# Kernel tuning notes

Measured on AMD Instinct MI355X. Metric: run time of the kernel, lower is better.

## Reference

```python
import jax, jax.numpy as jnp
import numpy as np

EMBED_DIM = 768
NUM_HEADS = 12
HEAD_DIM = EMBED_DIM // NUM_HEADS
SCALE = HEAD_DIM ** -0.5
B, S = 4, 2048


def setup_inputs() -> dict:
    key = jax.random.key(0)
    ks = jax.random.split(key, 9)
    w = 0.02
    return {
        "hidden_states": jax.random.normal(ks[0], (B, S, EMBED_DIM), jnp.float32),
        "Wq": jax.random.normal(ks[1], (EMBED_DIM, EMBED_DIM), jnp.float32) * w,
        "bq": jax.random.normal(ks[2], (EMBED_DIM,), jnp.float32) * w,
        "Wk": jax.random.normal(ks[3], (EMBED_DIM, EMBED_DIM), jnp.float32) * w,
        "bk": jax.random.normal(ks[4], (EMBED_DIM,), jnp.float32) * w,
        "Wv": jax.random.normal(ks[5], (EMBED_DIM, EMBED_DIM), jnp.float32) * w,
        "bv": jax.random.normal(ks[6], (EMBED_DIM,), jnp.float32) * w,
        "Wo": jax.random.normal(ks[7], (EMBED_DIM, EMBED_DIM), jnp.float32) * w,
        "bo": jax.random.normal(ks[8], (EMBED_DIM,), jnp.float32) * w,
    }


def reference(hidden_states, Wq, bq, Wk, bk, Wv, bv, Wo, bo):
    b, s, _ = hidden_states.shape
    # projections (torch Linear: x @ W.T + b)
    q = hidden_states @ Wq.T + bq
    k = hidden_states @ Wk.T + bk
    v = hidden_states @ Wv.T + bv
    # [b, h, s, d]
    q = q.reshape(b, s, NUM_HEADS, HEAD_DIM).transpose(0, 2, 1, 3)
    k = k.reshape(b, s, NUM_HEADS, HEAD_DIM).transpose(0, 2, 1, 3)
    v = v.reshape(b, s, NUM_HEADS, HEAD_DIM).transpose(0, 2, 1, 3)
    # full [b, h, s, s] attention matrix (faithful to the original, no fusion)
    attn_weights = jnp.einsum("bhqd,bhkd->bhqk", q, k) * SCALE
    attn_weights = jax.nn.softmax(attn_weights, axis=-1)
    attn_output = jnp.einsum("bhqk,bhkd->bhqd", attn_weights, v)
    attn_output = attn_output.transpose(0, 2, 1, 3).reshape(b, s, EMBED_DIM)
    attn_output = attn_output @ Wo.T + bo
    return attn_output, attn_weights
```

## Files before the change

kernel.cpp:

```cpp
#include <hip/hip_runtime.h>
#include <hip/hip_bf16.h>
#include <stdint.h>

#define EMBED 768
#define NH    12
#define HD    64
#define BB    4
#define SSEQ  2048
#define TOK   (BB*SSEQ)
#define ATT_SCALE 0.125f

typedef short  short8  __attribute__((ext_vector_type(8)));
typedef float  floatx4 __attribute__((ext_vector_type(4)));

__device__ __forceinline__ unsigned short f2bf(float f) {
  unsigned int u = __float_as_uint(f);
  return (unsigned short)((u + 0x7fffu + ((u >> 16) & 1u)) >> 16);
}

__device__ __forceinline__ void gl_lds16(const void* gsrc, void* ldst) {
  __builtin_amdgcn_global_load_lds(
      (__attribute__((address_space(1))) void*)(uintptr_t)gsrc,
      (__attribute__((address_space(3))) void*)ldst, 16, 0, 0);
}

__global__ void cvtk(const float* __restrict__ x, unsigned short* __restrict__ y, int n4) {
  int i = blockIdx.x * blockDim.x + threadIdx.x;
  if (i < n4) {
    float4 v = ((const float4*)x)[i];
    ushort4 o;
    o.x = f2bf(v.x); o.y = f2bf(v.y); o.z = f2bf(v.z); o.w = f2bf(v.w);
    ((ushort4*)y)[i] = o;
  }
}

__global__ __launch_bounds__(256, 2) void gemm_qkv(
    const unsigned short* __restrict__ Xb,
    const unsigned short* __restrict__ Wqb, const unsigned short* __restrict__ Wkb,
    const unsigned short* __restrict__ Wvb,
    const float* __restrict__ bq, const float* __restrict__ bk, const float* __restrict__ bv,
    unsigned short* __restrict__ Qw, unsigned short* __restrict__ Kw,
    unsigned short* __restrict__ Vw)
{
  __shared__ __align__(16) unsigned short As[128*64];
  __shared__ __align__(16) unsigned short Bs[128*64];
  const int z = blockIdx.z;
  const unsigned short* Wb = (z == 0) ? Wqb : (z == 1) ? Wkb : Wvb;
  const float* bias        = (z == 0) ? bq  : (z == 1) ? bk  : bv;
  unsigned short* Out      = (z == 0) ? Qw  : (z == 1) ? Kw  : Vw;

  const int tid = threadIdx.x;
  const int wid = tid >> 6, lane = tid & 63, quad = lane >> 4, l15 = lane & 15;
  const int wm = (wid >> 1) * 64, wn = (wid & 1) * 64;
  const int m0 = blockIdx.y * 128, n0 = blockIdx.x * 128;

  floatx4 acc[4][4] = {};

  for (int k0 = 0; k0 < EMBED; k0 += 64) {
#pragma unroll
    for (int p = 0; p < 4; ++p) {
      int f = p*256 + tid;
      int row = f >> 3, ch = f & 7;
      gl_lds16(Xb + (size_t)(m0+row)*EMBED + k0 + ch*8, &As[f*8]);
      gl_lds16(Wb + (size_t)(n0+row)*EMBED + k0 + ch*8, &Bs[f*8]);
    }
    __syncthreads();
#pragma unroll
    for (int kk = 0; kk < 2; ++kk) {
      short8 af[4], bf[4];
#pragma unroll
      for (int i = 0; i < 4; ++i)
        af[i] = *(const short8*)&As[(wm + i*16 + l15)*64 + kk*32 + quad*8];
#pragma unroll
      for (int j = 0; j < 4; ++j)
        bf[j] = *(const short8*)&Bs[(wn + j*16 + l15)*64 + kk*32 + quad*8];
#pragma unroll
      for (int i = 0; i < 4; ++i)
#pragma unroll
        for (int j = 0; j < 4; ++j)
          acc[i][j] = __builtin_amdgcn_mfma_f32_16x16x32_bf16(af[i], bf[j], acc[i][j], 0, 0, 0);
    }
    __syncthreads();
  }

#pragma unroll
  for (int j = 0; j < 4; ++j) {
    int n = n0 + wn + j*16 + l15;
    float bia = bias[n];
    int h = n >> 6, d = n & 63;
#pragma unroll
    for (int i = 0; i < 4; ++i) {
#pragma unroll
      for (int r = 0; r < 4; ++r) {
        int m = m0 + wm + i*16 + quad*4 + r;
        int b = m >> 11, s = m & 2047;
        Out[(size_t)(b*NH + h)*SSEQ*HD + (size_t)s*HD + d] = f2bf(acc[i][j][r] + bia);
      }
    }
  }
}

__global__ __launch_bounds__(256, 2) void gemm_o(
    const unsigned short* __restrict__ Ab, const unsigned short* __restrict__ Wb,
    const float* __restrict__ bias, float* __restrict__ Fo)
{
  __shared__ __align__(16) unsigned short As[128*64];
  __shared__ __align__(16) unsigned short Bs[128*64];
  const int tid = threadIdx.x;
  const int wid = tid >> 6, lane = tid & 63, quad = lane >> 4, l15 = lane & 15;
  const int wm = (wid >> 1) * 64, wn = (wid & 1) * 64;
  const int m0 = blockIdx.y * 128, n0 = blockIdx.x * 128;

  floatx4 acc[4][4] = {};

  for (int k0 = 0; k0 < EMBED; k0 += 64) {
#pragma unroll
    for (int p = 0; p < 4; ++p) {
      int f = p*256 + tid;
      int row = f >> 3, ch = f & 7;
      gl_lds16(Ab + (size_t)(m0+row)*EMBED + k0 + ch*8, &As[f*8]);
      gl_lds16(Wb + (size_t)(n0+row)*EMBED + k0 + ch*8, &Bs[f*8]);
    }
    __syncthreads();
#pragma unroll
    for (int kk = 0; kk < 2; ++kk) {
      short8 af[4], bf[4];
#pragma unroll
      for (int i = 0; i < 4; ++i)
        af[i] = *(const short8*)&As[(wm + i*16 + l15)*64 + kk*32 + quad*8];
#pragma unroll
      for (int j = 0; j < 4; ++j)
        bf[j] = *(const short8*)&Bs[(wn + j*16 + l15)*64 + kk*32 + quad*8];
#pragma unroll
      for (int i = 0; i < 4; ++i)
#pragma unroll
        for (int j = 0; j < 4; ++j)
          acc[i][j] = __builtin_amdgcn_mfma_f32_16x16x32_bf16(af[i], bf[j], acc[i][j], 0, 0, 0);
    }
    __syncthreads();
  }

#pragma unroll
  for (int j = 0; j < 4; ++j) {
    int n = n0 + wn + j*16 + l15;
    float bia = bias[n];
#pragma unroll
    for (int i = 0; i < 4; ++i) {
#pragma unroll
      for (int r = 0; r < 4; ++r) {
        int m = m0 + wm + i*16 + quad*4 + r;
        Fo[(size_t)m*EMBED + n] = acc[i][j][r] + bia;
      }
    }
  }
}

__global__ __launch_bounds__(256, 2) void attn(
    const unsigned short* __restrict__ Qw, const unsigned short* __restrict__ Kw,
    const unsigned short* __restrict__ Vw, unsigned short* __restrict__ AP,
    float* __restrict__ AWout)
{
  __shared__ __align__(16) unsigned short Qs[128*64];
  __shared__ __align__(16) unsigned short Ks[64*64];
  __shared__ __align__(16) unsigned short Vt[64*72];
  __shared__ __align__(16) unsigned short Ps[128*72];
  const int tid = threadIdx.x;
  const int wid = tid >> 6, lane = tid & 63, quad = lane >> 4, l15 = lane & 15;
  const int bh = blockIdx.x;
  const int q0 = blockIdx.y * 128;
  const unsigned short* Qh = Qw + (size_t)bh * SSEQ * HD;
  const unsigned short* Kh = Kw + (size_t)bh * SSEQ * HD;
  const unsigned short* Vh = Vw + (size_t)bh * SSEQ * HD;
  float* aw = AWout + (size_t)bh * SSEQ * SSEQ + (size_t)q0 * SSEQ;

#pragma unroll
  for (int p = 0; p < 4; ++p) {
    int f = p*256 + tid;
    gl_lds16(Qh + (size_t)(q0 + (f >> 3))*HD + (f & 7)*8, &Qs[f*8]);
  }

  float mi[2][4], li[2][4];
#pragma unroll
  for (int mf = 0; mf < 2; ++mf)
#pragma unroll
    for (int r = 0; r < 4; ++r) { mi[mf][r] = -1e30f; li[mf][r] = 0.f; }

  for (int kt = 0; kt < SSEQ/64; ++kt) {
    int k0 = kt * 64;
#pragma unroll
    for (int p = 0; p < 2; ++p) {
      int f = p*256 + tid;
      gl_lds16(Kh + (size_t)(k0 + (f >> 3))*HD + (f & 7)*8, &Ks[f*8]);
    }
    __syncthreads();

    floatx4 sa[2][4] = {};
#pragma unroll
    for (int kk = 0; kk < 2; ++kk) {
      short8 qf[2], kf[4];
#pragma unroll
      for (int mf = 0; mf < 2; ++mf)
        qf[mf] = *(const short8*)&Qs[(wid*32 + mf*16 + l15)*64 + kk*32 + quad*8];
#pragma unroll
      for (int nf = 0; nf < 4; ++nf)
        kf[nf] = *(const short8*)&Ks[(nf*16 + l15)*64 + kk*32 + quad*8];
#pragma unroll
      for (int mf = 0; mf < 2; ++mf)
#pragma unroll
        for (int nf = 0; nf < 4; ++nf)
          sa[mf][nf] = __builtin_amdgcn_mfma_f32_16x16x32_bf16(qf[mf], kf[nf], sa[mf][nf], 0, 0, 0);
    }
#pragma unroll
    for (int mf = 0; mf < 2; ++mf) {
#pragma unroll
      for (int r = 0; r < 4; ++r) {
        float s0 = sa[mf][0][r]*ATT_SCALE, s1 = sa[mf][1][r]*ATT_SCALE;
        float s2 = sa[mf][2][r]*ATT_SCALE, s3 = sa[mf][3][r]*ATT_SCALE;
        float tm = fmaxf(fmaxf(s0, s1), fmaxf(s2, s3));
#pragma unroll
        for (int msk = 1; msk < 16; msk <<= 1) tm = fmaxf(tm, __shfl_xor(tm, msk, 16));
        float mn = fmaxf(mi[mf][r], tm);
        float se = __expf(s0-mn) + __expf(s1-mn) + __expf(s2-mn) + __expf(s3-mn);
#pragma unroll
        for (int msk = 1; msk < 16; msk <<= 1) se += __shfl_xor(se, msk, 16);
        li[mf][r] = li[mf][r]*__expf(mi[mf][r]-mn) + se;
        mi[mf][r] = mn;
      }
    }
    __syncthreads();
  }

  float rli[2][4];
#pragma unroll
  for (int mf = 0; mf < 2; ++mf)
#pragma unroll
    for (int r = 0; r < 4; ++r) rli[mf][r] = 1.0f / li[mf][r];

  floatx4 oa[2][4] = {};
  for (int kt = 0; kt < SSEQ/64; ++kt) {
    int k0 = kt * 64;
#pragma unroll
    for (int p = 0; p < 2; ++p) {
      int f = p*256 + tid;
      gl_lds16(Kh + (size_t)(k0 + (f >> 3))*HD + (f & 7)*8, &Ks[f*8]);
    }
#pragma unroll
    for (int p = 0; p < 2; ++p) {
      int j = p*32 + (tid >> 3);
      int ch = tid & 7;
      short8 v = *(const short8*)&Vh[(size_t)(k0 + j)*HD + ch*8];
#pragma unroll
      for (int i = 0; i < 8; ++i)
        Vt[(ch*8 + i)*72 + j] = (unsigned short)v[i];
    }
    __syncthreads();

    floatx4 sa[2][4] = {};
#pragma unroll
    for (int kk = 0; kk < 2; ++kk) {
      short8 qf[2], kf[4];
#pragma unroll
      for (int mf = 0; mf < 2; ++mf)
        qf[mf] = *(const short8*)&Qs[(wid*32 + mf*16 + l15)*64 + kk*32 + quad*8];
#pragma unroll
      for (int nf = 0; nf < 4; ++nf)
        kf[nf] = *(const short8*)&Ks[(nf*16 + l15)*64 + kk*32 + quad*8];
#pragma unroll
      for (int mf = 0; mf < 2; ++mf)
#pragma unroll
        for (int nf = 0; nf < 4; ++nf)
          sa[mf][nf] = __builtin_amdgcn_mfma_f32_16x16x32_bf16(qf[mf], kf[nf], sa[mf][nf], 0, 0, 0);
    }

#pragma unroll
    for (int mf = 0; mf < 2; ++mf) {
#pragma unroll
      for (int nf = 0; nf < 4; ++nf) {
#pragma unroll
        for (int r = 0; r < 4; ++r) {
          float p = __expf(sa[mf][nf][r]*ATT_SCALE - mi[mf][r]) * rli[mf][r];
          int rl = wid*32 + mf*16 + quad*4 + r;
          aw[(size_t)rl*SSEQ + k0 + nf*16 + l15] = p;
          Ps[rl*72 + nf*16 + l15] = f2bf(p);
        }
      }
    }
#pragma unroll
    for (int kk = 0; kk < 2; ++kk) {
      short8 pf[2], vf[4];
#pragma unroll
      for (int mf = 0; mf < 2; ++mf)
        pf[mf] = *(const short8*)&Ps[(wid*32 + mf*16 + l15)*72 + kk*32 + quad*8];
#pragma unroll
      for (int nd = 0; nd < 4; ++nd)
        vf[nd] = *(const short8*)&Vt[(nd*16 + l15)*72 + kk*32 + quad*8];
#pragma unroll
      for (int mf = 0; mf < 2; ++mf)
#pragma unroll
        for (int nd = 0; nd < 4; ++nd)
          oa[mf][nd] = __builtin_amdgcn_mfma_f32_16x16x32_bf16(pf[mf], vf[nd], oa[mf][nd], 0, 0, 0);
    }
    __syncthreads();
  }

  const int b = bh / NH, h = bh % NH;
#pragma unroll
  for (int mf = 0; mf < 2; ++mf) {
#pragma unroll
    for (int nd = 0; nd < 4; ++nd) {
#pragma unroll
      for (int r = 0; r < 4; ++r) {
        int sq = q0 + wid*32 + mf*16 + quad*4 + r;
        int d  = nd*16 + l15;
        AP[(size_t)(b*SSEQ + sq)*EMBED + h*HD + d] = f2bf(oa[mf][nd][r]);
      }
    }
  }
}

extern "C" void kernel_launch(void* const* d_in, const int* in_sizes, int n_in,
                              void* d_out, int out_size, void* d_ws, size_t ws_size,
                              hipStream_t stream) {
  const float* X  = (const float*)d_in[0];
  const float* Wq = (const float*)d_in[1]; const float* bq = (const float*)d_in[2];
  const float* Wk = (const float*)d_in[3]; const float* bk = (const float*)d_in[4];
  const float* Wv = (const float*)d_in[5]; const float* bv = (const float*)d_in[6];
  const float* Wo = (const float*)d_in[7]; const float* bo = (const float*)d_in[8];

  float* outAttn = (float*)d_out;
  float* outW    = outAttn + (size_t)TOK * EMBED;

  const size_t XN = (size_t)TOK * EMBED;
  const size_t WN = (size_t)EMBED * EMBED;
  unsigned short* Xb  = (unsigned short*)d_ws;
  unsigned short* Wqb = Xb  + XN;
  unsigned short* Wkb = Wqb + WN;
  unsigned short* Wvb = Wkb + WN;
  unsigned short* Wob = Wvb + WN;
  unsigned short* Qws = Wob + WN;
  unsigned short* Kws = Qws + XN;
  unsigned short* Vws = Kws + XN;
  unsigned short* APs = Vws + XN;

  cvtk<<<dim3((unsigned)(XN/4/256)), 256, 0, stream>>>(X,  Xb,  (int)(XN/4));
  cvtk<<<dim3((unsigned)(WN/4/256)), 256, 0, stream>>>(Wq, Wqb, (int)(WN/4));
  cvtk<<<dim3((unsigned)(WN/4/256)), 256, 0, stream>>>(Wk, Wkb, (int)(WN/4));
  cvtk<<<dim3((unsigned)(WN/4/256)), 256, 0, stream>>>(Wv, Wvb, (int)(WN/4));
  cvtk<<<dim3((unsigned)(WN/4/256)), 256, 0, stream>>>(Wo, Wob, (int)(WN/4));

  gemm_qkv<<<dim3(EMBED/128, TOK/128, 3), 256, 0, stream>>>(
      Xb, Wqb, Wkb, Wvb, bq, bk, bv, Qws, Kws, Vws);

  attn<<<dim3(BB*NH, SSEQ/128), 256, 0, stream>>>(Qws, Kws, Vws, APs, outW);

  gemm_o<<<dim3(EMBED/128, TOK/128), 256, 0, stream>>>(APs, Wob, bo, outAttn);
}
```

Before: 1.152 ms.

## Double-buffer K/V tiles, keep Q in registers, pre-transpose V, defer softmax reductions

```diff
diff --git a/kernel.cpp b/kernel.cpp
--- a/kernel.cpp
+++ b/kernel.cpp
@@ -9,6 +9,7 @@
 #define SSEQ  2048
 #define TOK   (BB*SSEQ)
 #define ATT_SCALE 0.125f
+#define NT    (SSEQ/64)
 
 typedef short  short8  __attribute__((ext_vector_type(8)));
 typedef float  floatx4 __attribute__((ext_vector_type(4)));
@@ -23,6 +24,11 @@
       (__attribute__((address_space(1))) void*)(uintptr_t)gsrc,
       (__attribute__((address_space(3))) void*)ldst, 16, 0, 0);
 }
+
+#define VM_WAIT0()  asm volatile("s_waitcnt vmcnt(0)" ::: "memory")
+#define VM_WAIT32() asm volatile("s_waitcnt vmcnt(32)" ::: "memory")
+#define BARRIER()   asm volatile("s_barrier" ::: "memory")
+#define MEMFENCE()  asm volatile("" ::: "memory")
 
 __global__ void cvtk(const float* __restrict__ x, unsigned short* __restrict__ y, int n4) {
   int i = blockIdx.x * blockDim.x + threadIdx.x;
@@ -94,7 +100,10 @@
       for (int r = 0; r < 4; ++r) {
         int m = m0 + wm + i*16 + quad*4 + r;
         int b = m >> 11, s = m & 2047;
-        Out[(size_t)(b*NH + h)*SSEQ*HD + (size_t)s*HD + d] = f2bf(acc[i][j][r] + bia);
+        if (z == 2)
+          Out[((size_t)(b*NH + h)*HD + d)*SSEQ + s] = f2bf(acc[i][j][r] + bia);
+        else
+          Out[(size_t)(b*NH + h)*SSEQ*HD + (size_t)s*HD + d] = f2bf(acc[i][j][r] + bia);
       }
     }
   }
@@ -155,60 +164,67 @@
   }
 }
 
-__global__ __launch_bounds__(256, 2) void attn(
+__global__ __launch_bounds__(256, 3) void attn(
     const unsigned short* __restrict__ Qw, const unsigned short* __restrict__ Kw,
-    const unsigned short* __restrict__ Vw, unsigned short* __restrict__ AP,
+    const unsigned short* __restrict__ VTw, unsigned short* __restrict__ AP,
     float* __restrict__ AWout)
 {
-  __shared__ __align__(16) unsigned short Qs[128*64];
-  __shared__ __align__(16) unsigned short Ks[64*64];
-  __shared__ __align__(16) unsigned short Vt[64*72];
+  __shared__ __align__(16) unsigned short Ks[2][64*64];
+  __shared__ __align__(16) unsigned short Vt[2][64*64];
   __shared__ __align__(16) unsigned short Ps[128*72];
   const int tid = threadIdx.x;
   const int wid = tid >> 6, lane = tid & 63, quad = lane >> 4, l15 = lane & 15;
   const int bh = blockIdx.x;
   const int q0 = blockIdx.y * 128;
-  const unsigned short* Qh = Qw + (size_t)bh * SSEQ * HD;
-  const unsigned short* Kh = Kw + (size_t)bh * SSEQ * HD;
-  const unsigned short* Vh = Vw + (size_t)bh * SSEQ * HD;
+  const unsigned short* Qh  = Qw  + (size_t)bh * SSEQ * HD;
+  const unsigned short* Kh  = Kw  + (size_t)bh * SSEQ * HD;
+  const unsigned short* VTh = VTw + (size_t)bh * HD * SSEQ;
   float* aw = AWout + (size_t)bh * SSEQ * SSEQ + (size_t)q0 * SSEQ;
 
-#pragma unroll
-  for (int p = 0; p < 4; ++p) {
+  short8 qreg[2][2];
+#pragma unroll
+  for (int mf = 0; mf < 2; ++mf)
+#pragma unroll
+    for (int kk = 0; kk < 2; ++kk)
+      qreg[mf][kk] = *(const short8*)
+          &Qh[(size_t)(q0 + wid*32 + mf*16 + l15)*HD + kk*32 + quad*8];
+
+  float mi[2][4], li[2][4];
+#pragma unroll
+  for (int mf = 0; mf < 2; ++mf)
+#pragma unroll
+    for (int r = 0; r < 4; ++r) { mi[mf][r] = -1e30f; li[mf][r] = 0.f; }
+
+#pragma unroll
+  for (int p = 0; p < 2; ++p) {
     int f = p*256 + tid;
-    gl_lds16(Qh + (size_t)(q0 + (f >> 3))*HD + (f & 7)*8, &Qs[f*8]);
-  }
-
-  float mi[2][4], li[2][4];
-#pragma unroll
-  for (int mf = 0; mf < 2; ++mf)
-#pragma unroll
-    for (int r = 0; r < 4; ++r) { mi[mf][r] = -1e30f; li[mf][r] = 0.f; }
-
-  for (int kt = 0; kt < SSEQ/64; ++kt) {
-    int k0 = kt * 64;
-#pragma unroll
-    for (int p = 0; p < 2; ++p) {
-      int f = p*256 + tid;
-      gl_lds16(Kh + (size_t)(k0 + (f >> 3))*HD + (f & 7)*8, &Ks[f*8]);
-    }
-    __syncthreads();
+    gl_lds16(Kh + (size_t)(f >> 3)*HD + (f & 7)*8, &Ks[0][f*8]);
+  }
+  for (int kt = 0; kt < NT; ++kt) {
+    const int cur = kt & 1;
+    VM_WAIT0();
+    BARRIER();
+    if (kt + 1 < NT) {
+#pragma unroll
+      for (int p = 0; p < 2; ++p) {
+        int f = p*256 + tid;
+        gl_lds16(Kh + (size_t)((kt+1)*64 + (f >> 3))*HD + (f & 7)*8, &Ks[cur^1][f*8]);
+      }
+    }
+    MEMFENCE();
 
     floatx4 sa[2][4] = {};
 #pragma unroll
     for (int kk = 0; kk < 2; ++kk) {
-      short8 qf[2], kf[4];
+      short8 kf[4];
+#pragma unroll
+      for (int nf = 0; nf < 4; ++nf)
+        kf[nf] = *(const short8*)&Ks[cur][(nf*16 + l15)*64 + kk*32 + quad*8];
 #pragma unroll
       for (int mf = 0; mf < 2; ++mf)
-        qf[mf] = *(const short8*)&Qs[(wid*32 + mf*16 + l15)*64 + kk*32 + quad*8];
-#pragma unroll
-      for (int nf = 0; nf < 4; ++nf)
-        kf[nf] = *(const short8*)&Ks[(nf*16 + l15)*64 + kk*32 + quad*8];
-#pragma unroll
-      for (int mf = 0; mf < 2; ++mf)
 #pragma unroll
         for (int nf = 0; nf < 4; ++nf)
-          sa[mf][nf] = __builtin_amdgcn_mfma_f32_16x16x32_bf16(qf[mf], kf[nf], sa[mf][nf], 0, 0, 0);
+          sa[mf][nf] = __builtin_amdgcn_mfma_f32_16x16x32_bf16(qreg[mf][kk], kf[nf], sa[mf][nf], 0, 0, 0);
     }
 #pragma unroll
     for (int mf = 0; mf < 2; ++mf) {
@@ -217,59 +233,68 @@
         float s0 = sa[mf][0][r]*ATT_SCALE, s1 = sa[mf][1][r]*ATT_SCALE;
         float s2 = sa[mf][2][r]*ATT_SCALE, s3 = sa[mf][3][r]*ATT_SCALE;
         float tm = fmaxf(fmaxf(s0, s1), fmaxf(s2, s3));
-#pragma unroll
-        for (int msk = 1; msk < 16; msk <<= 1) tm = fmaxf(tm, __shfl_xor(tm, msk, 16));
-        float mn = fmaxf(mi[mf][r], tm);
-        float se = __expf(s0-mn) + __expf(s1-mn) + __expf(s2-mn) + __expf(s3-mn);
-#pragma unroll
-        for (int msk = 1; msk < 16; msk <<= 1) se += __shfl_xor(se, msk, 16);
-        li[mf][r] = li[mf][r]*__expf(mi[mf][r]-mn) + se;
+        float mo = mi[mf][r];
+        float mn = fmaxf(mo, tm);
+        float e0 = __expf(s0-mn), e1 = __expf(s1-mn);
+        float e2 = __expf(s2-mn), e3 = __expf(s3-mn);
+        li[mf][r] = li[mf][r]*__expf(mo-mn) + ((e0+e1)+(e2+e3));
         mi[mf][r] = mn;
       }
     }
-    __syncthreads();
   }
 
   float rli[2][4];
 #pragma unroll
-  for (int mf = 0; mf < 2; ++mf)
-#pragma unroll
-    for (int r = 0; r < 4; ++r) rli[mf][r] = 1.0f / li[mf][r];
+  for (int mf = 0; mf < 2; ++mf) {
+#pragma unroll
+    for (int r = 0; r < 4; ++r) {
+      float m = mi[mf][r], l = li[mf][r];
+#pragma unroll
+      for (int msk = 1; msk < 16; msk <<= 1) {
+        float om = __shfl_xor(m, msk, 16);
+        float ol = __shfl_xor(l, msk, 16);
+        float mn = fmaxf(m, om);
+        l = l*__expf(m-mn) + ol*__expf(om-mn);
+        m = mn;
+      }
+      mi[mf][r]  = m;
+      rli[mf][r] = 1.0f / l;
+    }
+  }
 
   floatx4 oa[2][4] = {};
-  for (int kt = 0; kt < SSEQ/64; ++kt) {
-    int k0 = kt * 64;
-#pragma unroll
-    for (int p = 0; p < 2; ++p) {
-      int f = p*256 + tid;
-      gl_lds16(Kh + (size_t)(k0 + (f >> 3))*HD + (f & 7)*8, &Ks[f*8]);
-    }
-#pragma unroll
-    for (int p = 0; p < 2; ++p) {
-      int j = p*32 + (tid >> 3);
-      int ch = tid & 7;
-      short8 v = *(const short8*)&Vh[(size_t)(k0 + j)*HD + ch*8];
-#pragma unroll
-      for (int i = 0; i < 8; ++i)
-        Vt[(ch*8 + i)*72 + j] = (unsigned short)v[i];
-    }
-    __syncthreads();
+#pragma unroll
+  for (int p = 0; p < 2; ++p) {
+    int f = p*256 + tid;
+    gl_lds16(Kh  + (size_t)(f >> 3)*HD + (f & 7)*8,   &Ks[0][f*8]);
+    gl_lds16(VTh + (size_t)(f >> 3)*SSEQ + (f & 7)*8, &Vt[0][f*8]);
+  }
+  for (int kt = 0; kt < NT; ++kt) {
+    const int cur = kt & 1;
+    if (kt == 0) { VM_WAIT0(); } else { VM_WAIT32(); }
+    BARRIER();
+    if (kt + 1 < NT) {
+#pragma unroll
+      for (int p = 0; p < 2; ++p) {
+        int f = p*256 + tid;
+        gl_lds16(Kh  + (size_t)((kt+1)*64 + (f >> 3))*HD + (f & 7)*8,       &Ks[cur^1][f*8]);
+        gl_lds16(VTh + (size_t)(f >> 3)*SSEQ + (kt+1)*64 + (f & 7)*8,       &Vt[cur^1][f*8]);
+      }
+    }
+    MEMFENCE();
 
     floatx4 sa[2][4] = {};
 #pragma unroll
     for (int kk = 0; kk < 2; ++kk) {
-      short8 qf[2], kf[4];
+      short8 kf[4];
+#pragma unroll
+      for (int nf = 0; nf < 4; ++nf)
+        kf[nf] = *(const short8*)&Ks[cur][(nf*16 + l15)*64 + kk*32 + quad*8];
 #pragma unroll
       for (int mf = 0; mf < 2; ++mf)
-        qf[mf] = *(const short8*)&Qs[(wid*32 + mf*16 + l15)*64 + kk*32 + quad*8];
-#pragma unroll
-      for (int nf = 0; nf < 4; ++nf)
-        kf[nf] = *(const short8*)&Ks[(nf*16 + l15)*64 + kk*32 + quad*8];
-#pragma unroll
-      for (int mf = 0; mf < 2; ++mf)
 #pragma unroll
         for (int nf = 0; nf < 4; ++nf)
-          sa[mf][nf] = __builtin_amdgcn_mfma_f32_16x16x32_bf16(qf[mf], kf[nf], sa[mf][nf], 0, 0, 0);
+          sa[mf][nf] = __builtin_amdgcn_mfma_f32_16x16x32_bf16(qreg[mf][kk], kf[nf], sa[mf][nf], 0, 0, 0);
     }
 
 #pragma unroll
@@ -280,11 +305,12 @@
         for (int r = 0; r < 4; ++r) {
           float p = __expf(sa[mf][nf][r]*ATT_SCALE - mi[mf][r]) * rli[mf][r];
           int rl = wid*32 + mf*16 + quad*4 + r;
-          aw[(size_t)rl*SSEQ + k0 + nf*16 + l15] = p;
+          aw[(size_t)rl*SSEQ + kt*64 + nf*16 + l15] = p;
           Ps[rl*72 + nf*16 + l15] = f2bf(p);
         }
       }
     }
+
 #pragma unroll
     for (int kk = 0; kk < 2; ++kk) {
       short8 pf[2], vf[4];
@@ -293,14 +319,13 @@
         pf[mf] = *(const short8*)&Ps[(wid*32 + mf*16 + l15)*72 + kk*32 + quad*8];
 #pragma unroll
       for (int nd = 0; nd < 4; ++nd)
-        vf[nd] = *(const short8*)&Vt[(nd*16 + l15)*72 + kk*32 + quad*8];
+        vf[nd] = *(const short8*)&Vt[cur][(nd*16 + l15)*64 + kk*32 + quad*8];
 #pragma unroll
       for (int mf = 0; mf < 2; ++mf)
 #pragma unroll
         for (int nd = 0; nd < 4; ++nd)
           oa[mf][nd] = __builtin_amdgcn_mfma_f32_16x16x32_bf16(pf[mf], vf[nd], oa[mf][nd], 0, 0, 0);
     }
-    __syncthreads();
   }
 
   const int b = bh / NH, h = bh % NH;
```

Result: faster. 1.054 ms (-8.5%).
